# Optimization experiments

Measured on AMD Instinct MI355X. Metric: run time of the kernel, lower is better.

The kernel has to match this reference:

```python
import jax, jax.numpy as jnp
import numpy as np

R = 5.0      # cutoff radius (init arg)
N = 4096     # total atoms
B = 8        # number of periodic systems in the batch


def setup_inputs() -> dict:
    key = jax.random.key(0)
    k1, k2, k3 = jax.random.split(key, 3)
    # positions in a ~20 Angstrom box (matches cell scale)
    pos = jax.random.uniform(k1, (N, 3), dtype=jnp.float32) * 20.0
    # sorted per-atom graph ids, as produced by a batched molecular loader
    batch = jnp.sort(jax.random.randint(k2, (N,), 0, B))
    # near-cubic 20A cells with small triclinic perturbation (well-conditioned)
    cell = jnp.eye(3, dtype=jnp.float32) * 20.0 + 0.5 * jax.random.normal(k3, (B, 3, 3), dtype=jnp.float32)
    return {"pos": pos, "cell": cell, "batch": batch}


def reference(pos, cell, batch):
    # Dense, fixed-shape equivalent of RadiusGraph.forward with PBC cell wrap.
    # Original returns dynamically filtered (edge_index, disp); here we return
    # the full [N,N,3] displacement grid (masked to 0 off-graph) plus the
    # boolean edge mask -- same math, jit-compatible static shapes.
    n = pos.shape[0]
    disp = pos[:, None, :] - pos[None, :, :]            # [N,N,3], row i minus col j
    # PBC minimum-image wrap: per edge, cell is taken from the ROW node's graph
    cell_n = cell[batch]                                # [N,3,3]
    inv_cellT = jnp.linalg.inv(jnp.swapaxes(cell_n, 1, 2))   # [N,3,3] = (cell^T)^{-1}
    # scaled = solve(cell^T, disp) vectorized over all pairs
    scaled = jnp.einsum('iab,ijb->ija', inv_cellT, disp)     # [N,N,3]
    disp = disp - jnp.einsum('iab,ijb->ija', cell_n, jnp.round(scaled))
    # edge validity: same graph, no self-loop, within cutoff (after wrap)
    same_graph = batch[:, None] == batch[None, :]
    not_self = ~jnp.eye(n, dtype=bool)
    mask = same_graph & not_self & (jnp.linalg.norm(disp, axis=-1) < R)
    disp = jnp.where(mask[..., None], disp, jnp.zeros((), disp.dtype))
    return disp, mask
```

## Files before the change

kernel.cpp:

```cpp
#include <hip/hip_runtime.h>
#include <math.h>

#define NATOMS 4096
#define R_CUT 5.0f
#define BLOCK 256
#define F4_PER_ROW (NATOMS / 4)
#define F4_PER_THREAD (F4_PER_ROW / BLOCK)

__device__ __forceinline__ int lower_bound_i(const int* __restrict__ b, int n, int v) {
    int lo = 0, hi = n;
    while (lo < hi) { int mid = (lo + hi) >> 1; if (b[mid] < v) lo = mid + 1; else hi = mid; }
    return lo;
}
__device__ __forceinline__ int upper_bound_i(const int* __restrict__ b, int n, int v) {
    int lo = 0, hi = n;
    while (lo < hi) { int mid = (lo + hi) >> 1; if (b[mid] <= v) lo = mid + 1; else hi = mid; }
    return lo;
}

__global__ __launch_bounds__(BLOCK) void radius_graph_sparse_kernel(
    const float* __restrict__ pos,
    const float* __restrict__ cell,
    const int*   __restrict__ batch,
    float* __restrict__ disp_out,
    float* __restrict__ mask_out)
{
    const int i   = blockIdx.x;
    const int tid = (int)threadIdx.x;

    const int bi = batch[i];
    const float pix = pos[i * 3 + 0];
    const float piy = pos[i * 3 + 1];
    const float piz = pos[i * 3 + 2];

    const float* C = cell + bi * 9;
    const float C00 = C[0], C01 = C[1], C02 = C[2];
    const float C10 = C[3], C11 = C[4], C12 = C[5];
    const float C20 = C[6], C21 = C[7], C22 = C[8];
    const float cof00 =  (C11 * C22 - C12 * C21);
    const float cof01 = -(C10 * C22 - C12 * C20);
    const float cof02 =  (C10 * C21 - C11 * C20);
    const float cof10 = -(C01 * C22 - C02 * C21);
    const float cof11 =  (C00 * C22 - C02 * C20);
    const float cof12 = -(C00 * C21 - C01 * C20);
    const float cof20 =  (C01 * C12 - C02 * C11);
    const float cof21 = -(C00 * C12 - C02 * C10);
    const float cof22 =  (C00 * C11 - C01 * C10);
    const float det = C00 * cof00 + C01 * cof01 + C02 * cof02;
    const float id  = 1.0f / det;
    const float A00 = cof00 * id, A01 = cof01 * id, A02 = cof02 * id;
    const float A10 = cof10 * id, A11 = cof11 * id, A12 = cof12 * id;
    const float A20 = cof20 * id, A21 = cof21 * id, A22 = cof22 * id;

    const int g0 = lower_bound_i(batch, NATOMS, bi);
    const int g1 = upper_bound_i(batch, NATOMS, bi);

    float* __restrict__ drow = disp_out + (size_t)i * (NATOMS * 3);
    float4* __restrict__ mrow = (float4*)(mask_out + (size_t)i * NATOMS);

    #pragma unroll
    for (int s = 0; s < F4_PER_THREAD; ++s) {
        const int f4 = tid + s * BLOCK;
        const int jbase = f4 * 4;
        float4 mv = make_float4(0.0f, 0.0f, 0.0f, 0.0f);

        if (jbase + 3 >= g0 && jbase < g1) {
            float* mvp = (float*)&mv;
            #pragma unroll
            for (int e = 0; e < 4; ++e) {
                const int j = jbase + e;
                if (j >= g0 && j < g1 && j != i) {
                    const float d0 = __fsub_rn(pix, pos[j * 3 + 0]);
                    const float d1 = __fsub_rn(piy, pos[j * 3 + 1]);
                    const float d2 = __fsub_rn(piz, pos[j * 3 + 2]);

                    const float s0 = __fadd_rn(__fadd_rn(__fmul_rn(A00, d0), __fmul_rn(A01, d1)), __fmul_rn(A02, d2));
                    const float s1 = __fadd_rn(__fadd_rn(__fmul_rn(A10, d0), __fmul_rn(A11, d1)), __fmul_rn(A12, d2));
                    const float s2 = __fadd_rn(__fadd_rn(__fmul_rn(A20, d0), __fmul_rn(A21, d1)), __fmul_rn(A22, d2));

                    const float r0 = rintf(s0);
                    const float r1 = rintf(s1);
                    const float r2 = rintf(s2);

                    const float w0 = __fsub_rn(d0, __fadd_rn(__fadd_rn(__fmul_rn(C00, r0), __fmul_rn(C01, r1)), __fmul_rn(C02, r2)));
                    const float w1 = __fsub_rn(d1, __fadd_rn(__fadd_rn(__fmul_rn(C10, r0), __fmul_rn(C11, r1)), __fmul_rn(C12, r2)));
                    const float w2 = __fsub_rn(d2, __fadd_rn(__fadd_rn(__fmul_rn(C20, r0), __fmul_rn(C21, r1)), __fmul_rn(C22, r2)));

                    const float n2 = __fadd_rn(__fadd_rn(__fmul_rn(w0, w0), __fmul_rn(w1, w1)), __fmul_rn(w2, w2));
                    if (sqrtf(n2) < R_CUT) {
                        mvp[e] = 1.0f;
                        drow[j * 3 + 0] = w0;
                        drow[j * 3 + 1] = w1;
                        drow[j * 3 + 2] = w2;
                    }
                }
            }
        }
        mrow[f4] = mv;
    }
}

extern "C" void kernel_launch(void* const* d_in, const int* in_sizes, int n_in,
                              void* d_out, int out_size, void* d_ws, size_t ws_size,
                              hipStream_t stream) {
    const float* pos   = (const float*)d_in[0];
    const float* cell  = (const float*)d_in[1];
    const int*   batch = (const int*)d_in[2];

    float* disp_out = (float*)d_out;
    float* mask_out = (float*)d_out + (size_t)NATOMS * NATOMS * 3;

    hipMemsetAsync(disp_out, 0, (size_t)NATOMS * NATOMS * 3 * sizeof(float), stream);

    radius_graph_sparse_kernel<<<NATOMS, BLOCK, 0, stream>>>(
        pos, cell, batch, disp_out, mask_out);
}
```

Measured before the change: 260.7 us.

## Write dense disp rows with coalesced float4 stores instead of memset plus scatter

Removes the separate full-buffer memset of the displacement output. The kernel now writes every disp element itself using coalesced float4 stores, computing two pair displacements per float4 to cover the 3-float stride. This avoids writing the large disp buffer twice and the scattered scalar stores. The cost is extra pair computations, since pairs are recomputed across neighbouring float4s and again for the mask.

```diff
diff --git a/kernel.cpp b/kernel.cpp
--- a/kernel.cpp
+++ b/kernel.cpp
@@ -4,8 +4,8 @@
 #define NATOMS 4096
 #define R_CUT 5.0f
 #define BLOCK 256
-#define F4_PER_ROW (NATOMS / 4)
-#define F4_PER_THREAD (F4_PER_ROW / BLOCK)
+#define DISP_F4_PER_ROW (NATOMS * 3 / 4)
+#define MASK_F4_PER_ROW (NATOMS / 4)
 
 __device__ __forceinline__ int lower_bound_i(const int* __restrict__ b, int n, int v) {
     int lo = 0, hi = n;
@@ -18,7 +18,42 @@
     return lo;
 }
 
-__global__ __launch_bounds__(BLOCK) void radius_graph_sparse_kernel(
+__device__ __forceinline__ void pair_disp(
+    int j, int i, int g0, int g1,
+    float pix, float piy, float piz,
+    const float* __restrict__ pos,
+    float A00, float A01, float A02, float A10, float A11, float A12,
+    float A20, float A21, float A22,
+    float C00, float C01, float C02, float C10, float C11, float C12,
+    float C20, float C21, float C22,
+    float& o0, float& o1, float& o2, bool& m)
+{
+    o0 = 0.0f; o1 = 0.0f; o2 = 0.0f; m = false;
+    if (j < g0 || j >= g1 || j == i) return;
+
+    const float d0 = __fsub_rn(pix, pos[j * 3 + 0]);
+    const float d1 = __fsub_rn(piy, pos[j * 3 + 1]);
+    const float d2 = __fsub_rn(piz, pos[j * 3 + 2]);
+
+    const float s0 = __fadd_rn(__fadd_rn(__fmul_rn(A00, d0), __fmul_rn(A01, d1)), __fmul_rn(A02, d2));
+    const float s1 = __fadd_rn(__fadd_rn(__fmul_rn(A10, d0), __fmul_rn(A11, d1)), __fmul_rn(A12, d2));
+    const float s2 = __fadd_rn(__fadd_rn(__fmul_rn(A20, d0), __fmul_rn(A21, d1)), __fmul_rn(A22, d2));
+
+    const float r0 = rintf(s0);
+    const float r1 = rintf(s1);
+    const float r2 = rintf(s2);
+
+    const float w0 = __fsub_rn(d0, __fadd_rn(__fadd_rn(__fmul_rn(C00, r0), __fmul_rn(C01, r1)), __fmul_rn(C02, r2)));
+    const float w1 = __fsub_rn(d1, __fadd_rn(__fadd_rn(__fmul_rn(C10, r0), __fmul_rn(C11, r1)), __fmul_rn(C12, r2)));
+    const float w2 = __fsub_rn(d2, __fadd_rn(__fadd_rn(__fmul_rn(C20, r0), __fmul_rn(C21, r1)), __fmul_rn(C22, r2)));
+
+    const float n2 = __fadd_rn(__fadd_rn(__fmul_rn(w0, w0), __fmul_rn(w1, w1)), __fmul_rn(w2, w2));
+    if (sqrtf(n2) < R_CUT) {
+        m = true; o0 = w0; o1 = w1; o2 = w2;
+    }
+}
+
+__global__ __launch_bounds__(BLOCK) void radius_graph_dense_kernel(
     const float* __restrict__ pos,
     const float* __restrict__ cell,
     const int*   __restrict__ batch,
@@ -55,48 +90,53 @@
     const int g0 = lower_bound_i(batch, NATOMS, bi);
     const int g1 = upper_bound_i(batch, NATOMS, bi);
 
-    float* __restrict__ drow = disp_out + (size_t)i * (NATOMS * 3);
+    float4* __restrict__ drow = (float4*)(disp_out + (size_t)i * (NATOMS * 3));
     float4* __restrict__ mrow = (float4*)(mask_out + (size_t)i * NATOMS);
 
+    #pragma unroll 4
+    for (int s = 0; s < DISP_F4_PER_ROW / BLOCK; ++s) {
+        const int f  = tid + s * BLOCK;
+        const int fb = f * 4;
+        const int j0 = fb / 3;
+        const int r  = fb - j0 * 3;
+        const int j1 = j0 + 1;
+
+        float4 v = make_float4(0.0f, 0.0f, 0.0f, 0.0f);
+        if (j1 >= g0 && j0 < g1) {
+            float a0, a1, a2, b0, b1, b2; bool ma, mb;
+            pair_disp(j0, i, g0, g1, pix, piy, piz, pos,
+                      A00, A01, A02, A10, A11, A12, A20, A21, A22,
+                      C00, C01, C02, C10, C11, C12, C20, C21, C22,
+                      a0, a1, a2, ma);
+            pair_disp(j1, i, g0, g1, pix, piy, piz, pos,
+                      A00, A01, A02, A10, A11, A12, A20, A21, A22,
+                      C00, C01, C02, C10, C11, C12, C20, C21, C22,
+                      b0, b1, b2, mb);
+            if (r == 0)      v = make_float4(a0, a1, a2, b0);
+            else if (r == 1) v = make_float4(a1, a2, b0, b1);
+            else             v = make_float4(a2, b0, b1, b2);
+        }
+        drow[f] = v;
+    }
+
     #pragma unroll
-    for (int s = 0; s < F4_PER_THREAD; ++s) {
-        const int f4 = tid + s * BLOCK;
-        const int jbase = f4 * 4;
+    for (int s = 0; s < MASK_F4_PER_ROW / BLOCK; ++s) {
+        const int f     = tid + s * BLOCK;
+        const int jbase = f * 4;
         float4 mv = make_float4(0.0f, 0.0f, 0.0f, 0.0f);
-
         if (jbase + 3 >= g0 && jbase < g1) {
             float* mvp = (float*)&mv;
             #pragma unroll
             for (int e = 0; e < 4; ++e) {
-                const int j = jbase + e;
-                if (j >= g0 && j < g1 && j != i) {
-                    const float d0 = __fsub_rn(pix, pos[j * 3 + 0]);
-                    const float d1 = __fsub_rn(piy, pos[j * 3 + 1]);
-                    const float d2 = __fsub_rn(piz, pos[j * 3 + 2]);
-
-                    const float s0 = __fadd_rn(__fadd_rn(__fmul_rn(A00, d0), __fmul_rn(A01, d1)), __fmul_rn(A02, d2));
-                    const float s1 = __fadd_rn(__fadd_rn(__fmul_rn(A10, d0), __fmul_rn(A11, d1)), __fmul_rn(A12, d2));
-                    const float s2 = __fadd_rn(__fadd_rn(__fmul_rn(A20, d0), __fmul_rn(A21, d1)), __fmul_rn(A22, d2));
-
-                    const float r0 = rintf(s0);
-                    const float r1 = rintf(s1);
-                    const float r2 = rintf(s2);
-
-                    const float w0 = __fsub_rn(d0, __fadd_rn(__fadd_rn(__fmul_rn(C00, r0), __fmul_rn(C01, r1)), __fmul_rn(C02, r2)));
-                    const float w1 = __fsub_rn(d1, __fadd_rn(__fadd_rn(__fmul_rn(C10, r0), __fmul_rn(C11, r1)), __fmul_rn(C12, r2)));
-                    const float w2 = __fsub_rn(d2, __fadd_rn(__fadd_rn(__fmul_rn(C20, r0), __fmul_rn(C21, r1)), __fmul_rn(C22, r2)));
-
-                    const float n2 = __fadd_rn(__fadd_rn(__fmul_rn(w0, w0), __fmul_rn(w1, w1)), __fmul_rn(w2, w2));
-                    if (sqrtf(n2) < R_CUT) {
-                        mvp[e] = 1.0f;
-                        drow[j * 3 + 0] = w0;
-                        drow[j * 3 + 1] = w1;
-                        drow[j * 3 + 2] = w2;
-                    }
-                }
+                float o0, o1, o2; bool m;
+                pair_disp(jbase + e, i, g0, g1, pix, piy, piz, pos,
+                          A00, A01, A02, A10, A11, A12, A20, A21, A22,
+                          C00, C01, C02, C10, C11, C12, C20, C21, C22,
+                          o0, o1, o2, m);
+                mvp[e] = m ? 1.0f : 0.0f;
             }
         }
-        mrow[f4] = mv;
+        mrow[f] = mv;
     }
 }
 
@@ -110,8 +150,6 @@
     float* disp_out = (float*)d_out;
     float* mask_out = (float*)d_out + (size_t)NATOMS * NATOMS * 3;
 
-    hipMemsetAsync(disp_out, 0, (size_t)NATOMS * NATOMS * 3 * sizeof(float), stream);
-
-    radius_graph_sparse_kernel<<<NATOMS, BLOCK, 0, stream>>>(
+    radius_graph_dense_kernel<<<NATOMS, BLOCK, 0, stream>>>(
         pos, cell, batch, disp_out, mask_out);
 }
```

Result: no change. 263.0 us (+0.9%).
